# Kernel tuning notes

Measured on AMD Instinct MI355X. Metric: run time of the kernel, lower is better.

The kernel has to match this reference:

```python
import jax, jax.numpy as jnp
import numpy as np
from jax import lax

V_TH = 1.0    # base firing threshold
RHO = 0.9     # adaptive-threshold decay
ADAPT = 0.1   # threshold increment per spike
SLOPE = 5.0   # surrogate-gradient sigmoid slope

@jax.custom_vjp
def spike_fn(v):
    return (v >= 0.0).astype(v.dtype)

def _spike_fwd(v):
    return spike_fn(v), v

def _spike_bwd(v, g):
    s = jax.nn.sigmoid(SLOPE * v)
    return (g * SLOPE * s * (1.0 - s),)

spike_fn.defvjp(_spike_fwd, _spike_bwd)

def lif_scan(x_seq, beta):
    # x_seq: (T, ..., F) channel-last; beta: (F,). Adaptive LIF with soft reset.
    def step(carry, x):
        mem, b = carry
        mem = beta * mem + x
        th = V_TH + b
        spk = spike_fn(mem - th)
        mem = mem - spk * th
        b = RHO * b + ADAPT * spk
        return (mem, b), spk
    z = jnp.zeros_like(x_seq[0])
    _, spikes = lax.scan(step, (z, z), x_seq)
    return spikes

def conv2d_s2(x, w, b):
    # NCHW conv, stride 2, padding 1
    y = lax.conv_general_dilated(x, w, (2, 2), ((1, 1), (1, 1)),
                                 dimension_numbers=('NCHW', 'OIHW', 'NCHW'))
    return y + b[None, :, None, None]

def mha(x, wq, wk, wv, wo, nh=4):
    B, T, D = x.shape
    dh = D // nh
    q = (x @ wq.T).reshape(B, T, nh, dh)
    k = (x @ wk.T).reshape(B, T, nh, dh)
    v = (x @ wv.T).reshape(B, T, nh, dh)
    att = jnp.einsum('bqhd,bkhd->bhqk', q, k) * (dh ** -0.5)
    p = jax.nn.softmax(att, axis=-1)
    o = jnp.einsum('bhqk,bkhd->bqhd', p, v).reshape(B, T, D)
    return o @ wo.T

def _forward(x, conv1_w, conv1_b, conv2_w, conv2_b, beta1, beta2,
             proj_w, proj_b, wq, wk, wv, wo, cls_w, cls_b):
    B, T, C, H, W = x.shape
    H1, W1, H2, W2 = H // 2, W // 2, H // 4, W // 4
    # stage 1 conv over all timesteps at once (conv is stateless)
    c1 = conv2d_s2(x.reshape(B * T, C, H, W), conv1_w, conv1_b)       # (B*T,16,H1,W1)
    c1 = jnp.moveaxis(c1.reshape(B, T, 16, H1, W1), 2, -1)            # (B,T,H1,W1,16)
    c1 = jnp.moveaxis(c1, 1, 0)                                       # (T,B,H1,W1,16)
    s1 = lif_scan(c1, beta1)                                          # (T,B,H1,W1,16)
    s1 = jnp.moveaxis(jnp.moveaxis(s1, 0, 1), -1, 2)                  # (B,T,16,H1,W1)
    # stage 2
    c2 = conv2d_s2(s1.reshape(B * T, 16, H1, W1), conv2_w, conv2_b)   # (B*T,32,H2,W2)
    c2 = jnp.moveaxis(c2.reshape(B, T, 32, H2, W2), 2, -1)
    c2 = jnp.moveaxis(c2, 1, 0)                                       # (T,B,H2,W2,32)
    s2 = lif_scan(c2, beta2)                                          # (T,B,H2,W2,32)
    total_spikes = s2.sum()
    # flatten channel-major to match torch permute(0,3,1,2).view(B,-1)
    feats = jnp.moveaxis(s2, -1, 2)                                   # (T,B,32,H2,W2)
    feats = jnp.moveaxis(feats, 0, 1).reshape(B, T, -1)               # (B,T,32*H2*W2)
    proj = feats @ proj_w.T + proj_b                                  # (B,T,64)
    attn = mha(proj, wq, wk, wv, wo)                                  # (B,T,64)
    context = attn.mean(axis=1)                                       # (B,64)
    # lif_out single step from zero state: mem = context
    spk_out = spike_fn(context - V_TH)
    logits = spk_out @ cls_w.T + cls_b
    sparsity = 1.0 - total_spikes / float(feats.size)
    return logits, sparsity

def setup_inputs() -> dict:
    key = jax.random.key(0)
    ks = jax.random.split(key, 10)
    B, T, C, H, W = 64, 8, 2, 128, 128
    D = 64
    flat = 32 * (H // 4) * (W // 4)  # 32768
    f = jnp.float32
    return {
        'x': (jax.random.uniform(ks[0], (B, T, C, H, W)) < 0.1).astype(f),  # sparse DVS events
        'conv1_w': jax.random.normal(ks[1], (16, C, 3, 3), f) * 0.2,
        'conv1_b': jnp.zeros((16,), f),
        'conv2_w': jax.random.normal(ks[2], (32, 16, 3, 3), f) * 0.1,
        'conv2_b': jnp.zeros((32,), f),
        'beta1': jnp.full((16,), 0.9, f),
        'beta2': jnp.full((32,), 0.9, f),
        'proj_w': jax.random.normal(ks[3], (D, flat), f) * (flat ** -0.5),
        'proj_b': jnp.zeros((D,), f),
        'wq': jax.random.normal(ks[4], (D, D), f) * (D ** -0.5),
        'wk': jax.random.normal(ks[5], (D, D), f) * (D ** -0.5),
        'wv': jax.random.normal(ks[6], (D, D), f) * (D ** -0.5),
        'wo': jax.random.normal(ks[7], (D, D), f) * (D ** -0.5),
        'cls_w': jax.random.normal(ks[8], (2, D), f) * (D ** -0.5),
        'cls_b': jnp.zeros((2,), f),
    }

def reference(x, conv1_w, conv1_b, conv2_w, conv2_b, beta1, beta2,
              proj_w, proj_b, wq, wk, wv, wo, cls_w, cls_b):
    return _forward(x, conv1_w, conv1_b, conv2_w, conv2_b, beta1, beta2,
                    proj_w, proj_b, wq, wk, wv, wo, cls_w, cls_b)
```

## Files before the change

### kernel.cpp

```cpp
#include <hip/hip_runtime.h>
#include <cstdint>

#define V_TH 1.0f
#define RHO 0.9f
#define ADAPT 0.1f

static constexpr int B = 64, T = 8, C = 2, H = 128, W = 128;
static constexpr int H1 = 64, W1 = 64;
static constexpr int H2 = 32, W2 = 32;
static constexpr int FLAT = 32 * H2 * W2;
static constexpr int R = B * T;

static constexpr size_t OFF_TRIP  = 0;
static constexpr size_t OFF_BITS  = OFF_TRIP + 8388608;
static constexpr size_t OFF_PWT   = OFF_BITS + 2097152;
static constexpr size_t OFF_CNT   = OFF_PWT + 8388608;
static constexpr size_t OFF_TBL   = OFF_CNT + 256;

__global__ __launch_bounds__(256) void k_mega1(
    const float* __restrict__ x, const float* __restrict__ w,
    const float* __restrict__ bias, const float* __restrict__ beta,
    uint64_t* __restrict__ trip,
    const float* __restrict__ pw, float* __restrict__ pwt,
    const float* __restrict__ c2w, float* __restrict__ tbl,
    unsigned int* __restrict__ cnt) {
  __shared__ float shmem[64 * 65];
  int bid = blockIdx.x;
  int tid = threadIdx.x;
  if (bid < 1024) {
    float* sw1 = shmem;
    for (int i = tid; i < 288; i += 256) {
      int c = i / 18, j = i % 18;
      sw1[j * 68 + c] = w[i];
    }
    __syncthreads();
    int gid = bid * 256 + tid;
    int w1 = gid & 63, h1 = (gid >> 6) & 63, b = gid >> 12;
    int lane = tid & 63;
    float bias_r[16], beta_r[16];
#pragma unroll
    for (int c = 0; c < 16; ++c) { bias_r[c] = bias[c]; beta_r[c] = beta[c]; }
    float mem[16], bth[16];
#pragma unroll
    for (int c = 0; c < 16; ++c) { mem[c] = 0.f; bth[c] = 0.f; }
    for (int t = 0; t < T; ++t) {
      int r = b * T + t;
      const float* xb = x + (size_t)(r * 2) * 16384;
      uint32_t M = 0;
#pragma unroll
      for (int ci = 0; ci < 2; ++ci) {
#pragma unroll
        for (int kh = 0; kh < 3; ++kh) {
          int y = 2 * h1 - 1 + kh;
          uint32_t w3 = 0;
          if (y >= 0 && y < H) {
            float2 v = *(const float2*)(xb + ci * 16384 + y * 128 + 2 * lane);
            float nl = __shfl(v.y, lane - 1, 64);
            uint32_t bl = (lane > 0 && nl != 0.f) ? 1u : 0u;
            uint32_t bm = (v.x != 0.f) ? 2u : 0u;
            uint32_t br = (v.y != 0.f) ? 4u : 0u;
            w3 = bl | bm | br;
          }
          M |= w3 << ((ci * 3 + kh) * 3);
        }
      }
      float acc[16];
#pragma unroll
      for (int c = 0; c < 16; ++c) acc[c] = bias_r[c];
      while (M) {
        int j = __ffs(M) - 1; M &= M - 1;
        const float4* wr = (const float4*)&sw1[j * 68];
        float4 a0 = wr[0], a1 = wr[1], a2 = wr[2], a3 = wr[3];
        acc[0] += a0.x; acc[1] += a0.y; acc[2] += a0.z; acc[3] += a0.w;
        acc[4] += a1.x; acc[5] += a1.y; acc[6] += a1.z; acc[7] += a1.w;
        acc[8] += a2.x; acc[9] += a2.y; acc[10] += a2.z; acc[11] += a2.w;
        acc[12] += a3.x; acc[13] += a3.y; acc[14] += a3.z; acc[15] += a3.w;
      }
      uint32_t mask = 0;
#pragma unroll
      for (int c = 0; c < 16; ++c) {
        mem[c] = beta_r[c] * mem[c] + acc[c];
        float th = V_TH + bth[c];
        bool s = (mem[c] >= th);
        if (s) { mem[c] -= th; mask |= (1u << c); }
        bth[c] = RHO * bth[c] + (s ? ADAPT : 0.f);
      }
      int iL = 2 * lane - 1; if (iL < 0) iL = 0;
      uint32_t mL = __shfl((int)mask, iL, 64);
      uint32_t mC = __shfl((int)mask, 2 * lane, 64);
      uint32_t mR = __shfl((int)mask, 2 * lane + 1, 64);
      if (lane < 32) {
        uint64_t tw = (uint64_t)(lane ? mL : 0u) | ((uint64_t)mC << 16) |
                      ((uint64_t)mR << 32);
        trip[(size_t)(r * H1 + h1) * 32 + lane] = tw;
      }
    }
  } else if (bid < 1536) {
    float* tile = shmem;
    int tb = bid - 1024;
    int c = tb >> 4, pt = tb & 15;
    int posc = ((c & 3) << 3) + (c >> 2);
    int p0 = pt * 64;
    int lane = tid & 63, quad = tid >> 6;
#pragma unroll
    for (int it = 0; it < 16; ++it) {
      int d = it * 4 + quad;
      tile[d * 65 + lane] = pw[(size_t)d * FLAT + c * 1024 + p0 + lane];
    }
    __syncthreads();
#pragma unroll
    for (int it = 0; it < 16; ++it) {
      int pp = it * 4 + quad;
      pwt[((size_t)((p0 + pp) * 32 + posc)) * 64 + lane] = tile[lane * 65 + pp];
    }
  } else if (bid == 1536) {
    if (tid == 0) *cnt = 0u;
  } else {
    int kb = bid - 1537;
    int kh = kb / 6, bp = kb % 6;
    int v = tid;
    float e[32];
#pragma unroll
    for (int co = 0; co < 32; ++co) e[co] = 0.f;
    for (int i = 0; i < 8; ++i) {
      if ((v >> i) & 1) {
        int j = bp * 8 + i;
        int kw = j >> 4, ci = j & 15;
#pragma unroll
        for (int co = 0; co < 32; ++co)
          e[co] += c2w[((co * 16 + ci) * 3 + kh) * 3 + kw];
      }
    }
#pragma unroll
    for (int co = 0; co < 32; ++co) tbl[((size_t)(kb * 256 + v)) * 32 + co] = e[co];
  }
}

__global__ __launch_bounds__(256) void k_conv2_lif2(
    const uint64_t* __restrict__ trip, const float* __restrict__ tbl,
    const float* __restrict__ bias, const float* __restrict__ beta,
    uint32_t* __restrict__ bits, unsigned int* __restrict__ cnt) {
  __shared__ unsigned int sc;
  int tid = threadIdx.x;
  if (tid == 0) sc = 0u;
  __syncthreads();
  int lane = tid & 63;
  int li = lane & 7;
  int p8 = lane >> 3;
  int wvi = (blockIdx.x * 256 + tid) >> 6;
  int px = wvi * 8 + p8;
  int w2 = px & 31, h2 = (px >> 5) & 31, b = px >> 10;
  float4 b4 = *(const float4*)&bias[4 * li];
  float4 bt4 = *(const float4*)&beta[4 * li];
  float m0v = 0.f, m1v = 0.f, m2v = 0.f, m3v = 0.f;
  float t0 = 0.f, t1 = 0.f, t2 = 0.f, t3 = 0.f;
  unsigned int lc = 0;
  const float4* tb4 = (const float4*)tbl;
  for (int t = 0; t < T; ++t) {
    int r = b * T + t;
    const uint64_t* tr = trip + (size_t)(r * 64 + 2 * h2) * 32 + w2;
    uint64_t q0 = (h2 > 0) ? tr[-32] : 0ull;
    uint64_t q1 = tr[0];
    uint64_t q2 = tr[32];
    uint32_t r0l = (uint32_t)q0, r0h = (uint32_t)(q0 >> 32);
    uint32_t r1l = (uint32_t)q1, r1h = (uint32_t)(q1 >> 32);
    uint32_t r2l = (uint32_t)q2, r2h = (uint32_t)(q2 >> 32);
    float a0 = b4.x, a1 = b4.y, a2 = b4.z, a3 = b4.w;
#define LOOK(g, word, sh) { uint32_t by = ((word) >> (sh)) & 255u;            \
    float4 wv = tb4[((g) << 11) + (by << 3) + li];                            \
    a0 += wv.x; a1 += wv.y; a2 += wv.z; a3 += wv.w; }
    LOOK(0, r0l, 0) LOOK(1, r0l, 8) LOOK(2, r0l, 16) LOOK(3, r0l, 24)
    LOOK(4, r0h, 0) LOOK(5, r0h, 8)
    LOOK(6, r1l, 0) LOOK(7, r1l, 8) LOOK(8, r1l, 16) LOOK(9, r1l, 24)
    LOOK(10, r1h, 0) LOOK(11, r1h, 8)
    LOOK(12, r2l, 0) LOOK(13, r2l, 8) LOOK(14, r2l, 16) LOOK(15, r2l, 24)
    LOOK(16, r2h, 0) LOOK(17, r2h, 8)
#undef LOOK
    m0v = bt4.x * m0v + a0;
    m1v = bt4.y * m1v + a1;
    m2v = bt4.z * m2v + a2;
    m3v = bt4.w * m3v + a3;
    float th0 = V_TH + t0, th1 = V_TH + t1, th2 = V_TH + t2, th3 = V_TH + t3;
    bool s0 = (m0v >= th0), s1 = (m1v >= th1), s2 = (m2v >= th2), s3 = (m3v >= th3);
    if (s0) m0v -= th0;
    if (s1) m1v -= th1;
    if (s2) m2v -= th2;
    if (s3) m3v -= th3;
    t0 = RHO * t0 + (s0 ? ADAPT : 0.f);
    t1 = RHO * t1 + (s1 ? ADAPT : 0.f);
    t2 = RHO * t2 + (s2 ? ADAPT : 0.f);
    t3 = RHO * t3 + (s3 ? ADAPT : 0.f);
    unsigned long long bl0 = __ballot(s0);
    unsigned long long bl1 = __ballot(s1);
    unsigned long long bl2 = __ballot(s2);
    unsigned long long bl3 = __ballot(s3);
    if (li == 0) {
      int sh = p8 * 8;
      uint32_t m32 = ((uint32_t)(bl0 >> sh) & 0xFFu)
                   | (((uint32_t)(bl1 >> sh) & 0xFFu) << 8)
                   | (((uint32_t)(bl2 >> sh) & 0xFFu) << 16)
                   | (((uint32_t)(bl3 >> sh) & 0xFFu) << 24);
      bits[(size_t)r * 1024 + (px & 1023)] = m32;
      lc += __popc(m32);
    }
  }
  if (li == 0) atomicAdd(&sc, lc);
  __syncthreads();
  if (tid == 0) atomicAdd(cnt, sc);
}

__global__ __launch_bounds__(256) void k_proj_gemm(
    const uint32_t* __restrict__ bits, const float* __restrict__ pwt,
    float* __restrict__ partial) {
  int rt = blockIdx.x >> 4;
  int ks = (blockIdx.x & 15) * 4 + (threadIdx.x >> 6);
  int d = threadIdx.x & 63;
  float acc[8] = {0, 0, 0, 0, 0, 0, 0, 0};
  const uint32_t* bb = bits + (size_t)rt * 8 * 1024;
  for (int wi = 0; wi < 16; ++wi) {
    int word = ks * 16 + wi;
    const float* rowbase = pwt + ((size_t)word * 32) * 64 + d;
#pragma unroll
    for (int ri = 0; ri < 8; ++ri) {
      uint32_t m = bb[ri * 1024 + word];
      while (m) {
        int c = __ffs(m) - 1; m &= m - 1;
        acc[ri] += rowbase[c << 6];
      }
    }
  }
#pragma unroll
  for (int ri = 0; ri < 8; ++ri)
    partial[((size_t)(rt * 64 + ks) * 8 + ri) * 64 + d] = acc[ri];
}

__global__ __launch_bounds__(256) void k_attn_final(
    const float* __restrict__ partial, const float* __restrict__ pb,
    const float* __restrict__ wq, const float* __restrict__ wk,
    const float* __restrict__ wv, const float* __restrict__ wo,
    const float* __restrict__ clsw, const float* __restrict__ clsb,
    const unsigned int* __restrict__ cnt, float* __restrict__ out) {
  __shared__ float swq[64 * 65], swk[64 * 65], swv[64 * 65], swo[64 * 65];
  __shared__ float sp[8 * 65], sq[8 * 65], sk[8 * 65], sv[8 * 65], so2[8 * 65];
  __shared__ float satt[4][8][8];
  __shared__ float sob[64];
  int b = blockIdx.x, tid = threadIdx.x;
  for (int i = tid; i < 4096; i += 256) {
    int dd = i >> 6, e = i & 63;
    swq[dd * 65 + e] = wq[i]; swk[dd * 65 + e] = wk[i];
    swv[dd * 65 + e] = wv[i]; swo[dd * 65 + e] = wo[i];
  }
  for (int i = tid; i < 512; i += 256) {
    int ri = i >> 6, d = i & 63;
    float s = pb[d];
    const float* p = partial + ((size_t)(b * 64) * 8 + ri) * 64 + d;
#pragma unroll
    for (int ks = 0; ks < 64; ++ks) s += p[(size_t)ks * 512];
    sp[ri * 65 + d] = s;
  }
  __syncthreads();
#pragma unroll
  for (int p = 0; p < 2; ++p) {
    int idx = p * 256 + tid, t = idx >> 6, d = idx & 63;
    float qa = 0.f, ka = 0.f, va = 0.f;
    for (int e = 0; e < 64; ++e) {
      float pe = sp[t * 65 + e];
      qa += pe * swq[d * 65 + e];
      ka += pe * swk[d * 65 + e];
      va += pe * swv[d * 65 + e];
    }
    sq[t * 65 + d] = qa; sk[t * 65 + d] = ka; sv[t * 65 + d] = va;
  }
  __syncthreads();
  {
    int h = tid >> 6, q = (tid >> 3) & 7, k = tid & 7;
    float s = 0.f;
    for (int j = 0; j < 16; ++j)
      s += sq[q * 65 + h * 16 + j] * sk[k * 65 + h * 16 + j];
    satt[h][q][k] = s * 0.25f;
  }
  __syncthreads();
  if (tid < 32) {
    int h = tid >> 3, q2 = tid & 7;
    float m = -1e30f;
    for (int k2 = 0; k2 < 8; ++k2) m = fmaxf(m, satt[h][q2][k2]);
    float sum = 0.f;
    for (int k2 = 0; k2 < 8; ++k2) {
      float e = expf(satt[h][q2][k2] - m);
      satt[h][q2][k2] = e; sum += e;
    }
    float inv = 1.f / sum;
    for (int k2 = 0; k2 < 8; ++k2) satt[h][q2][k2] *= inv;
  }
  __syncthreads();
#pragma unroll
  for (int p = 0; p < 2; ++p) {
    int idx = p * 256 + tid, t = idx >> 6, d = idx & 63;
    int h = d >> 4;
    float o = 0.f;
    for (int k = 0; k < 8; ++k) o += satt[h][t][k] * sv[k * 65 + d];
    so2[t * 65 + d] = o;
  }
  __syncthreads();
  if (tid < 64) {
    float ob = 0.f;
    for (int t = 0; t < 8; ++t) ob += so2[t * 65 + tid];
    sob[tid] = ob * 0.125f;
  }
  __syncthreads();
  if (tid < 64) {
    float ctx = 0.f;
    for (int e = 0; e < 64; ++e) ctx += sob[e] * swo[tid * 65 + e];
    int spk = (ctx >= V_TH) ? 1 : 0;
    unsigned long long ball = __ballot(spk);
    if (tid < 2) {
      float lg = clsb[tid];
      for (int dd = 0; dd < 64; ++dd)
        if ((ball >> dd) & 1ull) lg += clsw[tid * 64 + dd];
      out[b * 2 + tid] = lg;
    }
    if (b == 0 && tid == 2)
      out[128] = 1.f - (float)(*cnt) / 16777216.f;
  }
}

extern "C" void kernel_launch(void* const* d_in, const int* in_sizes, int n_in,
                              void* d_out, int out_size, void* d_ws, size_t ws_size,
                              hipStream_t stream) {
  const float* x    = (const float*)d_in[0];
  const float* c1w  = (const float*)d_in[1];
  const float* c1b  = (const float*)d_in[2];
  const float* c2w  = (const float*)d_in[3];
  const float* c2b  = (const float*)d_in[4];
  const float* bt1  = (const float*)d_in[5];
  const float* bt2  = (const float*)d_in[6];
  const float* pw   = (const float*)d_in[7];
  const float* pb   = (const float*)d_in[8];
  const float* wq   = (const float*)d_in[9];
  const float* wk   = (const float*)d_in[10];
  const float* wv   = (const float*)d_in[11];
  const float* wo   = (const float*)d_in[12];
  const float* clsw = (const float*)d_in[13];
  const float* clsb = (const float*)d_in[14];
  float* out = (float*)d_out;

  uint8_t* ws = (uint8_t*)d_ws;
  uint64_t* trip  = (uint64_t*)(ws + OFF_TRIP);
  float*    part  = (float*)(ws + OFF_TRIP);
  uint32_t* bits  = (uint32_t*)(ws + OFF_BITS);
  float*    pwt   = (float*)(ws + OFF_PWT);
  unsigned int* cnt = (unsigned int*)(ws + OFF_CNT);
  float*    tbl   = (float*)(ws + OFF_TBL);

  k_mega1<<<1555, 256, 0, stream>>>(x, c1w, c1b, bt1, trip, pw, pwt, c2w, tbl, cnt);
  k_conv2_lif2<<<2048, 256, 0, stream>>>(trip, tbl, c2b, bt2, bits, cnt);
  k_proj_gemm<<<1024, 256, 0, stream>>>(bits, pwt, part);
  k_attn_final<<<64, 256, 0, stream>>>(part, pb, wq, wk, wv, wo, clsw, clsb, cnt, out);
}
```

Before: 224.9 us.

## Stage conv1 input rows in LDS and double proj GEMM k-split blocks

The conv1+LIF1 part of k_mega1 now has each block cover four output rows of one batch. For every timestep it stages the nine overlapping input rows per channel into shared memory, so neighbouring waves share row loads instead of each doing its own global float2 loads with shuffles. This adds two barriers per timestep. The projection GEMM splits the K dimension twice as finely (2048 blocks, 8 words each) to expose more parallelism. That doubles the partial sums written to a new, separate workspace region and the reduction work in the attention kernel.

```diff
diff --git a/kernel.cpp b/kernel.cpp
--- a/kernel.cpp
+++ b/kernel.cpp
@@ -16,6 +16,7 @@
 static constexpr size_t OFF_PWT   = OFF_BITS + 2097152;
 static constexpr size_t OFF_CNT   = OFF_PWT + 8388608;
 static constexpr size_t OFF_TBL   = OFF_CNT + 256;
+static constexpr size_t OFF_PART  = OFF_TBL + 2359296;
 
 __global__ __launch_bounds__(256) void k_mega1(
     const float* __restrict__ x, const float* __restrict__ w,
@@ -29,39 +30,45 @@
   int tid = threadIdx.x;
   if (bid < 1024) {
     float* sw1 = shmem;
+    float* sx = shmem + 1280;
     for (int i = tid; i < 288; i += 256) {
       int c = i / 18, j = i % 18;
       sw1[j * 68 + c] = w[i];
     }
-    __syncthreads();
-    int gid = bid * 256 + tid;
-    int w1 = gid & 63, h1 = (gid >> 6) & 63, b = gid >> 12;
-    int lane = tid & 63;
+    int b = bid >> 4;
+    int h0 = (bid & 15) * 4;
+    int wv = tid >> 6, lane = tid & 63;
     float bias_r[16], beta_r[16];
 #pragma unroll
     for (int c = 0; c < 16; ++c) { bias_r[c] = bias[c]; beta_r[c] = beta[c]; }
     float mem[16], bth[16];
 #pragma unroll
     for (int c = 0; c < 16; ++c) { mem[c] = 0.f; bth[c] = 0.f; }
+    int ylo = 2 * h0 - 1;
     for (int t = 0; t < T; ++t) {
       int r = b * T + t;
       const float* xb = x + (size_t)(r * 2) * 16384;
+      __syncthreads();
+      for (int i = tid; i < 2304; i += 256) {
+        int ci = i >> 11;
+        int rem = i - ci * 1152;
+        ci = i / 1152; rem = i % 1152;
+        int row = rem >> 7, col = rem & 127;
+        int y = ylo + row;
+        sx[i] = (y >= 0 && y < H) ? xb[ci * 16384 + y * 128 + col] : 0.f;
+      }
+      __syncthreads();
       uint32_t M = 0;
 #pragma unroll
       for (int ci = 0; ci < 2; ++ci) {
 #pragma unroll
         for (int kh = 0; kh < 3; ++kh) {
-          int y = 2 * h1 - 1 + kh;
-          uint32_t w3 = 0;
-          if (y >= 0 && y < H) {
-            float2 v = *(const float2*)(xb + ci * 16384 + y * 128 + 2 * lane);
-            float nl = __shfl(v.y, lane - 1, 64);
-            uint32_t bl = (lane > 0 && nl != 0.f) ? 1u : 0u;
-            uint32_t bm = (v.x != 0.f) ? 2u : 0u;
-            uint32_t br = (v.y != 0.f) ? 4u : 0u;
-            w3 = bl | bm | br;
-          }
-          M |= w3 << ((ci * 3 + kh) * 3);
+          int row = 2 * wv + kh;
+          const float* rp = &sx[ci * 1152 + row * 128 + 2 * lane];
+          uint32_t bl = (lane > 0 && rp[-1] != 0.f) ? 1u : 0u;
+          uint32_t bm = (rp[0] != 0.f) ? 2u : 0u;
+          uint32_t br = (rp[1] != 0.f) ? 4u : 0u;
+          M |= (bl | bm | br) << ((ci * 3 + kh) * 3);
         }
       }
       float acc[16];
@@ -85,6 +92,7 @@
         if (s) { mem[c] -= th; mask |= (1u << c); }
         bth[c] = RHO * bth[c] + (s ? ADAPT : 0.f);
       }
+      int h1 = h0 + wv;
       int iL = 2 * lane - 1; if (iL < 0) iL = 0;
       uint32_t mL = __shfl((int)mask, iL, 64);
       uint32_t mC = __shfl((int)mask, 2 * lane, 64);
@@ -212,13 +220,13 @@
 __global__ __launch_bounds__(256) void k_proj_gemm(
     const uint32_t* __restrict__ bits, const float* __restrict__ pwt,
     float* __restrict__ partial) {
-  int rt = blockIdx.x >> 4;
-  int ks = (blockIdx.x & 15) * 4 + (threadIdx.x >> 6);
+  int wid = blockIdx.x * 4 + (threadIdx.x >> 6);
+  int rt = wid >> 7, ks2 = wid & 127;
   int d = threadIdx.x & 63;
   float acc[8] = {0, 0, 0, 0, 0, 0, 0, 0};
   const uint32_t* bb = bits + (size_t)rt * 8 * 1024;
-  for (int wi = 0; wi < 16; ++wi) {
-    int word = ks * 16 + wi;
+  for (int wi = 0; wi < 8; ++wi) {
+    int word = ks2 * 8 + wi;
     const float* rowbase = pwt + ((size_t)word * 32) * 64 + d;
 #pragma unroll
     for (int ri = 0; ri < 8; ++ri) {
@@ -231,7 +239,7 @@
   }
 #pragma unroll
   for (int ri = 0; ri < 8; ++ri)
-    partial[((size_t)(rt * 64 + ks) * 8 + ri) * 64 + d] = acc[ri];
+    partial[((size_t)(rt * 128 + ks2) * 8 + ri) * 64 + d] = acc[ri];
 }
 
 __global__ __launch_bounds__(256) void k_attn_final(
@@ -253,9 +261,9 @@
   for (int i = tid; i < 512; i += 256) {
     int ri = i >> 6, d = i & 63;
     float s = pb[d];
-    const float* p = partial + ((size_t)(b * 64) * 8 + ri) * 64 + d;
-#pragma unroll
-    for (int ks = 0; ks < 64; ++ks) s += p[(size_t)ks * 512];
+    const float* p = partial + ((size_t)(b * 128) * 8 + ri) * 64 + d;
+#pragma unroll
+    for (int ks2 = 0; ks2 < 128; ++ks2) s += p[(size_t)ks2 * 512];
     sp[ri * 65 + d] = s;
   }
   __syncthreads();
@@ -346,14 +354,14 @@
 
   uint8_t* ws = (uint8_t*)d_ws;
   uint64_t* trip  = (uint64_t*)(ws + OFF_TRIP);
-  float*    part  = (float*)(ws + OFF_TRIP);
   uint32_t* bits  = (uint32_t*)(ws + OFF_BITS);
   float*    pwt   = (float*)(ws + OFF_PWT);
   unsigned int* cnt = (unsigned int*)(ws + OFF_CNT);
   float*    tbl   = (float*)(ws + OFF_TBL);
+  float*    part  = (float*)(ws + OFF_PART);
 
   k_mega1<<<1555, 256, 0, stream>>>(x, c1w, c1b, bt1, trip, pw, pwt, c2w, tbl, cnt);
   k_conv2_lif2<<<2048, 256, 0, stream>>>(trip, tbl, c2b, bt2, bits, cnt);
-  k_proj_gemm<<<1024, 256, 0, stream>>>(bits, pwt, part);
+  k_proj_gemm<<<2048, 256, 0, stream>>>(bits, pwt, part);
   k_attn_final<<<64, 256, 0, stream>>>(part, pb, wq, wk, wv, wo, clsw, clsb, cnt, out);
 }
```

Result: slower. 242.9 us (+8.0%).
